# Kernel optimization log

Hardware: AMD Instinct MI355X
Metric: run time of the kernel (lower is better)

The kernel has to match this reference:

```python
import jax, jax.numpy as jnp
import numpy as np

B, D, H, W, T, C = 2, 16, 16, 16, 16, 96
NH = 4                      # num_heads
WS = (4, 4, 4, 4)           # window size
SS = (2, 2, 2, 2)           # shift size
EPS = 1e-5
HIDDEN = 4 * C


def _compute_mask():
    # Standard Swin shifted-window attention mask, extended to 4D.
    img = np.zeros((D, H, W, T), np.float32)
    sl = [[slice(0, -WS[i]), slice(-WS[i], -SS[i]), slice(-SS[i], None)] for i in range(4)]
    cnt = 0
    for a in sl[0]:
        for b in sl[1]:
            for c in sl[2]:
                for d in sl[3]:
                    img[a, b, c, d] = cnt
                    cnt += 1
    x = img.reshape(D // WS[0], WS[0], H // WS[1], WS[1], W // WS[2], WS[2], T // WS[3], WS[3])
    x = x.transpose(0, 2, 4, 6, 1, 3, 5, 7).reshape(-1, WS[0] * WS[1] * WS[2] * WS[3])
    diff = x[:, None, :] - x[:, :, None]
    return np.where(diff != 0, np.float32(-100.0), np.float32(0.0))


def setup_inputs() -> dict:
    key = jax.random.key(0)
    ks = jax.random.split(key, 6)
    w = lambda k, shape: jax.random.normal(k, shape, jnp.float32) * 0.02
    return {
        'x': jax.random.normal(ks[0], (B, D, H, W, T, C), jnp.float32),
        'mask_matrix': jnp.asarray(_compute_mask()),
        'norm1_g': jnp.ones((C,), jnp.float32), 'norm1_b': jnp.zeros((C,), jnp.float32),
        'qkv_w': w(ks[1], (3 * C, C)), 'qkv_b': jnp.zeros((3 * C,), jnp.float32),
        'proj_w': w(ks[2], (C, C)), 'proj_b': jnp.zeros((C,), jnp.float32),
        'norm2_g': jnp.ones((C,), jnp.float32), 'norm2_b': jnp.zeros((C,), jnp.float32),
        'fc1_w': w(ks[3], (HIDDEN, C)), 'fc1_b': jnp.zeros((HIDDEN,), jnp.float32),
        'fc2_w': w(ks[4], (C, HIDDEN)), 'fc2_b': jnp.zeros((C,), jnp.float32),
    }


def _ln(x, g, b):
    mu = jnp.mean(x, -1, keepdims=True)
    var = jnp.var(x, -1, keepdims=True)
    return (x - mu) * jax.lax.rsqrt(var + EPS) * g + b


def _partition(x):
    # (B, D, H, W, T, C) -> (B*nw, N, C)
    b, c = x.shape[0], x.shape[-1]
    x = x.reshape(b, D // WS[0], WS[0], H // WS[1], WS[1], W // WS[2], WS[2], T // WS[3], WS[3], c)
    x = x.transpose(0, 1, 3, 5, 7, 2, 4, 6, 8, 9)
    return x.reshape(-1, WS[0] * WS[1] * WS[2] * WS[3], c)


def _reverse(win, b):
    c = win.shape[-1]
    x = win.reshape(b, D // WS[0], H // WS[1], W // WS[2], T // WS[3], WS[0], WS[1], WS[2], WS[3], c)
    x = x.transpose(0, 1, 5, 2, 6, 3, 7, 4, 8, 9)
    return x.reshape(b, D, H, W, T, c)


def reference(x, mask_matrix, norm1_g, norm1_b, qkv_w, qkv_b, proj_w, proj_b,
              norm2_g, norm2_b, fc1_w, fc1_b, fc2_w, fc2_b):
    b, c = x.shape[0], x.shape[-1]
    hd = c // NH
    scale = hd ** -0.5
    shortcut = x
    # norm -> (no pad needed: dims divisible by window) -> cyclic shift
    xn = _ln(x, norm1_g, norm1_b)
    xs = jnp.roll(xn, shift=(-SS[0], -SS[1], -SS[2], -SS[3]), axis=(1, 2, 3, 4))
    win = _partition(xs)                              # (B_, N, C)
    B_, N, _ = win.shape
    qkv = (win @ qkv_w.T + qkv_b).reshape(B_, N, 3, NH, hd).transpose(2, 0, 3, 1, 4)
    q, k, v = qkv[0] * scale, qkv[1], qkv[2]          # (B_, NH, N, hd)
    attn = jnp.einsum('bhid,bhjd->bhij', q, k)        # (B_, NH, N, N)
    nw = mask_matrix.shape[0]
    attn = attn.reshape(B_ // nw, nw, NH, N, N) + mask_matrix[None, :, None]
    attn = jax.nn.softmax(attn.reshape(B_, NH, N, N), axis=-1)
    out = jnp.einsum('bhij,bhjd->bhid', attn, v)
    out = out.transpose(0, 2, 1, 3).reshape(B_, N, c)
    out = out @ proj_w.T + proj_b
    xr = _reverse(out, b)
    xr = jnp.roll(xr, shift=SS, axis=(1, 2, 3, 4))    # reverse cyclic shift
    x = shortcut + xr
    # MLP block
    h = _ln(x, norm2_g, norm2_b)
    h = jax.nn.gelu(h @ fc1_w.T + fc1_b, approximate=False)
    return x + (h @ fc2_w.T + fc2_b)
```

## Files before the change

kernel.cpp:

```cpp
#include <hip/hip_runtime.h>

#define TOK   131072
#define BWIN  512

typedef __attribute__((ext_vector_type(8))) short bf16x8;
typedef __attribute__((ext_vector_type(4))) float f32x4;

__device__ __forceinline__ unsigned short f2us(float f) {
  union { float f; unsigned int i; } x; x.f = f;
  return (unsigned short)((x.i + 0x7fffu + ((x.i >> 16) & 1u)) >> 16);
}
__device__ __forceinline__ unsigned cvtpk(float lo, float hi) {
  unsigned r;
  asm("v_cvt_pk_bf16_f32 %0, %1, %2" : "=v"(r) : "v"(lo), "v"(hi));
  return r;
}

#define IW1   0
#define IW2   36864
#define IQKV  73728
#define IPROJ 104448
#define IMG_SHORTS 116736

__global__ __launch_bounds__(256) void k_prepw(
    const float* __restrict__ fc1_w, const float* __restrict__ fc2_w,
    const float* __restrict__ qkv_w, const float* __restrict__ proj_w,
    unsigned short* __restrict__ img) {
  int i = blockIdx.x * 256 + threadIdx.x;
  const int l = (i >> 3) & 63, j = i & 7;
  const int quad = l >> 4, l15 = l & 15;
  float v = 0.f;
  if (i < 36864) {
    int f = i >> 9; int nc = f / 18, rem = f - nc * 18;
    int ks = rem / 6, nt = rem - ks * 6;
    v = fc1_w[(size_t)(nc * 96 + nt * 16 + l15) * 96 + ks * 32 + quad * 8 + j];
  } else if (i < 73728) {
    int f = (i - 36864) >> 9; int nc = f / 18, rem = f - nc * 18;
    int ks = rem / 6, nt = rem - ks * 6;
    v = fc2_w[(size_t)(nt * 16 + l15) * 384 + nc * 96 + ks * 32 + quad * 8 + j];
  } else if (i < 104448) {
    int f = (i - 73728) >> 9; int h = f / 15, rem = f - h * 15;
    int ks = rem / 5, mt = rem - ks * 5;
    int e = mt * 16 + l15;
    if (e < 72) {
      int grp = e / 24, rr = e - grp * 24;
      v = qkv_w[(size_t)(grp * 96 + h * 24 + rr) * 96 + ks * 32 + quad * 8 + j];
    }
  } else {
    int f = (i - 104448) >> 9; int h = f / 6, nt = f - h * 6;
    int e = quad * 8 + j;
    if (e < 24) v = proj_w[(size_t)(nt * 16 + l15) * 96 + h * 24 + e];
  }
  img[i] = f2us(v);
}

__global__ __launch_bounds__(256) void k_ln1(const float* __restrict__ x,
                                             const float* __restrict__ g,
                                             const float* __restrict__ b,
                                             unsigned short* __restrict__ xn) {
  const int wave = threadIdx.x >> 6, lane = threadIdx.x & 63;
  const int t = blockIdx.x * 4 + wave;
  const int b_ = t >> 8, n = t & 255;
  const int batch = b_ >> 8, wi = b_ & 255;
  const int wd = (wi >> 6) & 3, wh = (wi >> 4) & 3, ww = (wi >> 2) & 3, wt = wi & 3;
  const int aa = (n >> 6) & 3, bb = (n >> 4) & 3, cc = (n >> 2) & 3, dd = n & 3;
  const int sd = (wd * 4 + aa + 2) & 15, sh = (wh * 4 + bb + 2) & 15;
  const int sw = (ww * 4 + cc + 2) & 15, st = (wt * 4 + dd + 2) & 15;
  const size_t gg = ((((size_t)(batch * 16 + sd) * 16 + sh) * 16 + sw) * 16 + st);

  float2 f;
  if (lane < 48) f = *(const float2*)(x + gg * 96 + 2 * lane);
  else { f.x = 0.f; f.y = 0.f; }
  float s = f.x + f.y, q2 = f.x * f.x + f.y * f.y;
  #pragma unroll
  for (int m = 1; m < 64; m <<= 1) { s += __shfl_xor(s, m, 64); q2 += __shfl_xor(q2, m, 64); }
  const float mu = s * (1.f / 96.f);
  const float var = q2 * (1.f / 96.f) - mu * mu;
  const float rs = rsqrtf(fmaxf(var, 0.f) + 1e-5f);
  if (lane < 48) {
    float a0 = (f.x - mu) * rs * g[2 * lane]     + b[2 * lane];
    float a1 = (f.y - mu) * rs * g[2 * lane + 1] + b[2 * lane + 1];
    ((unsigned int*)xn)[(size_t)t * 48 + lane] = cvtpk(a0, a1);
  }
}

#define O_K   10240
#define O_VT  20480
#define O_U   28928
#define O_LB  37632
#define LDS_BYTES 75520

__global__ __launch_bounds__(256, 2) void k_win(
    const unsigned short* __restrict__ xn, const float* __restrict__ x,
    const unsigned short* __restrict__ img,
    const float* __restrict__ qkv_b, const float* __restrict__ proj_b,
    float* __restrict__ out) {
  extern __shared__ short lds[];
  short* s_q  = lds;
  short* s_k  = lds + O_K;
  short* s_vt = lds + O_VT;
  short* s_u  = lds + O_U;
  unsigned char* s_lb = (unsigned char*)(lds + O_LB);

  const int tid = threadIdx.x;
  const int w = tid >> 6, l = tid & 63, quad = l >> 4, l15 = l & 15;
  const int q0 = w * 64;
  const int b_ = blockIdx.x;
  const int batch = b_ >> 8, wi = b_ & 255;
  const int wd = (wi >> 6) & 3, wh = (wi >> 4) & 3, ww = (wi >> 2) & 3, wt = wi & 3;
  const float scale = 0.20412414523193154f;
  const f32x4 fz = {0.f, 0.f, 0.f, 0.f};

  {
    const int n = tid;
    const int aa = (n >> 6) & 3, bb = (n >> 4) & 3, cc = (n >> 2) & 3, dd = n & 3;
    const int p0 = wd * 4 + aa, p1 = wh * 4 + bb, p2 = ww * 4 + cc, p3 = wt * 4 + dd;
    const int r0 = p0 >= 14 ? 2 : (p0 >= 12 ? 1 : 0);
    const int r1 = p1 >= 14 ? 2 : (p1 >= 12 ? 1 : 0);
    const int r2 = p2 >= 14 ? 2 : (p2 >= 12 ? 1 : 0);
    const int r3 = p3 >= 14 ? 2 : (p3 >= 12 ? 1 : 0);
    s_lb[n] = (unsigned char)(((r0 * 3 + r1) * 3 + r2) * 3 + r3);
    unsigned int* qp = (unsigned int*)(s_q + n * 40 + 24);
    unsigned int* kp = (unsigned int*)(s_k + n * 40 + 24);
    #pragma unroll
    for (int i = 0; i < 8; i++) { qp[i] = 0u; kp[i] = 0u; }
    unsigned int* vz = (unsigned int*)(s_vt + 24 * 264);
    for (int i = tid; i < 8 * 132; i += 256)
      vz[i] = (i < 132) ? 0x3f803f80u : 0u;
  }
  __syncthreads();

  unsigned lj4[16];
  #pragma unroll
  for (int km = 0; km < 16; km++)
    lj4[km] = *(const unsigned*)&s_lb[km * 16 + quad * 4];

  f32x4 pacc[4][6];
  #pragma unroll
  for (int mt = 0; mt < 4; mt++)
    #pragma unroll
    for (int nt = 0; nt < 6; nt++) pacc[mt][nt] = fz;

  const unsigned short* xw = xn + (size_t)b_ * 256 * 96;
  const unsigned short* wq = img + IQKV;
  const unsigned short* wp = img + IPROJ;

  for (int h = 0; h < 4; h++) {
    f32x4 acc[5][4];
    #pragma unroll
    for (int mt = 0; mt < 5; mt++)
      #pragma unroll
      for (int nt = 0; nt < 4; nt++) acc[mt][nt] = fz;
    #pragma unroll
    for (int ks = 0; ks < 3; ks++) {
      bf16x8 aw[5];
      #pragma unroll
      for (int mt = 0; mt < 5; mt++)
        aw[mt] = *(const bf16x8*)(wq + ((h * 3 + ks) * 5 + mt) * 512 + l * 8);
      #pragma unroll
      for (int nt = 0; nt < 4; nt++) {
        bf16x8 bx = *(const bf16x8*)(xw + (size_t)(q0 + nt * 16 + l15) * 96 + ks * 32 + quad * 8);
        #pragma unroll
        for (int mt = 0; mt < 5; mt++)
          acc[mt][nt] = __builtin_amdgcn_mfma_f32_16x16x32_bf16(aw[mt], bx, acc[mt][nt], 0, 0, 0);
      }
    }
    #pragma unroll
    for (int mt = 0; mt < 5; mt++) {
      const int e0 = mt * 16 + quad * 4;
      #pragma unroll
      for (int nt = 0; nt < 4; nt++) {
        const int tok = q0 + nt * 16 + l15;
        if (e0 < 24) {
          uint2 pk;
          pk.x = cvtpk((acc[mt][nt][0] + qkv_b[h * 24 + e0]) * scale,
                       (acc[mt][nt][1] + qkv_b[h * 24 + e0 + 1]) * scale);
          pk.y = cvtpk((acc[mt][nt][2] + qkv_b[h * 24 + e0 + 2]) * scale,
                       (acc[mt][nt][3] + qkv_b[h * 24 + e0 + 3]) * scale);
          *(uint2*)&s_q[tok * 40 + e0] = pk;
        } else if (e0 < 48) {
          const int e = e0 - 24;
          uint2 pk;
          pk.x = cvtpk(acc[mt][nt][0] + qkv_b[96 + h * 24 + e],
                       acc[mt][nt][1] + qkv_b[96 + h * 24 + e + 1]);
          pk.y = cvtpk(acc[mt][nt][2] + qkv_b[96 + h * 24 + e + 2],
                       acc[mt][nt][3] + qkv_b[96 + h * 24 + e + 3]);
          *(uint2*)&s_k[tok * 40 + e] = pk;
        } else if (e0 < 72) {
          const int e = e0 - 48;
          #pragma unroll
          for (int r = 0; r < 4; r++)
            s_vt[(e + r) * 264 + tok] = (short)f2us(acc[mt][nt][r] + qkv_b[192 + h * 24 + e + r]);
        }
      }
    }
    __syncthreads();
    short* s_p = s_u + w * 2176;
    #pragma unroll 1
    for (int mt4 = 0; mt4 < 4; mt4++) {
      const int qt0 = q0 + mt4 * 16;
      f32x4 sc[16];
      #pragma unroll
      for (int km = 0; km < 16; km++) sc[km] = fz;
      bf16x8 bq = *(const bf16x8*)&s_q[(qt0 + l15) * 40 + quad * 8];
      __builtin_amdgcn_s_setprio(1);
      #pragma unroll
      for (int km = 0; km < 16; km++) {
        bf16x8 ak = *(const bf16x8*)&s_k[(km * 16 + l15) * 40 + quad * 8];
        sc[km] = __builtin_amdgcn_mfma_f32_16x16x32_bf16(ak, bq, sc[km], 0, 0, 0);
      }
      __builtin_amdgcn_s_setprio(0);
      const unsigned lq = s_lb[qt0 + l15];
      f32x4 ov[2] = {fz, fz};
      #pragma unroll
      for (int half = 0; half < 2; half++) {
        asm volatile("s_waitcnt lgkmcnt(0)" ::: "memory");
        #pragma unroll
        for (int km = half * 8; km < half * 8 + 8; km++) {
          unsigned lj = lj4[km];
          float p0 = ((lj & 255u)         == lq) ? __expf(sc[km][0]) : 0.f;
          float p1 = (((lj >> 8) & 255u)  == lq) ? __expf(sc[km][1]) : 0.f;
          float p2 = (((lj >> 16) & 255u) == lq) ? __expf(sc[km][2]) : 0.f;
          float p3 = ((lj >> 24)          == lq) ? __expf(sc[km][3]) : 0.f;
          uint2 pk;
          pk.x = cvtpk(p0, p1);
          pk.y = cvtpk(p2, p3);
          *(uint2*)&s_p[l15 * 136 + (km - half * 8) * 16 + quad * 4] = pk;
        }
        asm volatile("s_waitcnt lgkmcnt(0)" ::: "memory");
        __builtin_amdgcn_s_setprio(1);
        #pragma unroll
        for (int ks = 0; ks < 4; ks++) {
          bf16x8 bp = *(const bf16x8*)&s_p[l15 * 136 + ks * 32 + quad * 8];
          #pragma unroll
          for (int vm = 0; vm < 2; vm++) {
            bf16x8 av = *(const bf16x8*)&s_vt[(vm * 16 + l15) * 264 + half * 128 + ks * 32 + quad * 8];
            ov[vm] = __builtin_amdgcn_mfma_f32_16x16x32_bf16(av, bp, ov[vm], 0, 0, 0);
          }
        }
        __builtin_amdgcn_s_setprio(0);
      }
      float rsum = __shfl(ov[1][0], 32 + l15, 64);
      float inv = 1.f / rsum;
      uint2 o0;
      o0.x = cvtpk(ov[0][0] * inv, ov[0][1] * inv);
      o0.y = cvtpk(ov[0][2] * inv, ov[0][3] * inv);
      *(uint2*)&s_q[(qt0 + l15) * 40 + quad * 4] = o0;
      if (quad < 2) {
        uint2 o1;
        o1.x = cvtpk(ov[1][0] * inv, ov[1][1] * inv);
        o1.y = cvtpk(ov[1][2] * inv, ov[1][3] * inv);
        *(uint2*)&s_q[(qt0 + l15) * 40 + 16 + quad * 4] = o1;
      }
    }
    {
      bf16x8 bp[6];
      #pragma unroll
      for (int nt = 0; nt < 6; nt++)
        bp[nt] = *(const bf16x8*)(wp + (h * 6 + nt) * 512 + l * 8);
      #pragma unroll
      for (int mt = 0; mt < 4; mt++) {
        bf16x8 ao = *(const bf16x8*)&s_q[(q0 + mt * 16 + l15) * 40 + quad * 8];
        #pragma unroll
        for (int nt = 0; nt < 6; nt++)
          pacc[mt][nt] = __builtin_amdgcn_mfma_f32_16x16x32_bf16(ao, bp[nt], pacc[mt][nt], 0, 0, 0);
      }
    }
    __syncthreads();
  }

  #pragma unroll
  for (int mt = 0; mt < 4; mt++) {
    #pragma unroll
    for (int r = 0; r < 4; r++) {
      int n = q0 + mt * 16 + quad * 4 + r;
      const int aa = (n >> 6) & 3, bb = (n >> 4) & 3, cc = (n >> 2) & 3, dd = n & 3;
      const int sd = (wd * 4 + aa + 2) & 15, sh = (wh * 4 + bb + 2) & 15;
      const int sw = (ww * 4 + cc + 2) & 15, st = (wt * 4 + dd + 2) & 15;
      const size_t gg = ((((size_t)(batch * 16 + sd) * 16 + sh) * 16 + sw) * 16 + st);
      #pragma unroll
      for (int nt = 0; nt < 6; nt++) {
        int c = nt * 16 + l15;
        out[gg * 96 + c] = x[gg * 96 + c] + proj_b[c] + pacc[mt][nt][r];
      }
    }
  }
}

__global__ __launch_bounds__(256, 3) void k_mlp(
    float* __restrict__ io,
    const float* __restrict__ n2g, const float* __restrict__ n2b,
    const unsigned short* __restrict__ img,
    const float* __restrict__ fc1_b, const float* __restrict__ fc2_b) {
  __shared__ __align__(16) short s_a[128 * 104];
  __shared__ __align__(16) short s_h[128 * 104];

  const int tid = threadIdx.x;
  const int w = tid >> 6, l = tid & 63;
  const int quad = l >> 4, l15 = l & 15;
  const size_t t0 = (size_t)blockIdx.x * 128;
  const f32x4 fz = {0.f, 0.f, 0.f, 0.f};

  {
    const int r = tid >> 1, hf = tid & 1;
    const float4* base = (const float4*)(io + (t0 + r) * 96 + hf * 48);
    float v[48];
    float s = 0.f, q = 0.f;
    #pragma unroll
    for (int j = 0; j < 12; j++) {
      float4 f = base[j];
      v[4 * j] = f.x; v[4 * j + 1] = f.y; v[4 * j + 2] = f.z; v[4 * j + 3] = f.w;
      s += f.x + f.y + f.z + f.w;
      q += f.x * f.x + f.y * f.y + f.z * f.z + f.w * f.w;
    }
    s += __shfl_xor(s, 1); q += __shfl_xor(q, 1);
    const float mu = s * (1.f / 96.f);
    const float var = q * (1.f / 96.f) - mu * mu;
    const float rs = rsqrtf(fmaxf(var, 0.f) + 1e-5f);
    unsigned int* row = (unsigned int*)&s_a[r * 104] + hf * 24;
    #pragma unroll
    for (int jj = 0; jj < 24; jj++) {
      int k0 = hf * 48 + 2 * jj;
      float lo = (v[2 * jj]     - mu) * rs * n2g[k0]     + n2b[k0];
      float hi = (v[2 * jj + 1] - mu) * rs * n2g[k0 + 1] + n2b[k0 + 1];
      row[jj] = cvtpk(lo, hi);
    }
  }

  f32x4 acc2[2][6];
  #pragma unroll
  for (int m = 0; m < 2; m++)
    #pragma unroll
    for (int i = 0; i < 6; i++) acc2[m][i] = fz;

  for (int nc = 0; nc < 4; nc++) {
    f32x4 acc1[2][6];
    #pragma unroll
    for (int m = 0; m < 2; m++)
      #pragma unroll
      for (int i = 0; i < 6; i++) acc1[m][i] = fz;
    #pragma unroll
    for (int ks = 0; ks < 3; ks++) {
      bf16x8 bw[6];
      #pragma unroll
      for (int nt = 0; nt < 6; nt++)
        bw[nt] = *(const bf16x8*)(img + IW1 + ((nc * 3 + ks) * 6 + nt) * 512 + l * 8);
      #pragma unroll
      for (int m = 0; m < 2; m++) {
        bf16x8 af = *(const bf16x8*)&s_a[(w * 32 + m * 16 + l15) * 104 + ks * 32 + quad * 8];
        #pragma unroll
        for (int nt = 0; nt < 6; nt++)
          acc1[m][nt] = __builtin_amdgcn_mfma_f32_16x16x32_bf16(af, bw[nt], acc1[m][nt], 0, 0, 0);
      }
    }
    #pragma unroll
    for (int m = 0; m < 2; m++)
      #pragma unroll
      for (int nt = 0; nt < 6; nt++) {
        int col = nt * 16 + l15;
        float bv = fc1_b[nc * 96 + col];
        #pragma unroll
        for (int r = 0; r < 4; r++) {
          float z = acc1[m][nt][r] + bv;
          float g = 0.5f * z * (1.f + erff(z * 0.70710678118654752f));
          s_h[(w * 32 + m * 16 + quad * 4 + r) * 104 + col] = (short)f2us(g);
        }
      }
    #pragma unroll
    for (int ks = 0; ks < 3; ks++) {
      bf16x8 bw[6];
      #pragma unroll
      for (int nt = 0; nt < 6; nt++)
        bw[nt] = *(const bf16x8*)(img + IW2 + ((nc * 3 + ks) * 6 + nt) * 512 + l * 8);
      #pragma unroll
      for (int m = 0; m < 2; m++) {
        bf16x8 af = *(const bf16x8*)&s_h[(w * 32 + m * 16 + l15) * 104 + ks * 32 + quad * 8];
        #pragma unroll
        for (int nt = 0; nt < 6; nt++)
          acc2[m][nt] = __builtin_amdgcn_mfma_f32_16x16x32_bf16(af, bw[nt], acc2[m][nt], 0, 0, 0);
      }
    }
  }

  #pragma unroll
  for (int m = 0; m < 2; m++)
    #pragma unroll
    for (int nt = 0; nt < 6; nt++) {
      int col = nt * 16 + l15;
      float bv = fc2_b[col];
      #pragma unroll
      for (int r = 0; r < 4; r++) {
        size_t idx = (t0 + w * 32 + m * 16 + quad * 4 + r) * 96 + col;
        io[idx] = io[idx] + acc2[m][nt][r] + bv;
      }
    }
}

extern "C" void kernel_launch(void* const* d_in, const int* in_sizes, int n_in,
                              void* d_out, int out_size, void* d_ws, size_t ws_size,
                              hipStream_t stream) {
  const float* x      = (const float*)d_in[0];
  const float* n1g    = (const float*)d_in[2];
  const float* n1b    = (const float*)d_in[3];
  const float* qkv_w  = (const float*)d_in[4];
  const float* qkv_b  = (const float*)d_in[5];
  const float* proj_w = (const float*)d_in[6];
  const float* proj_b = (const float*)d_in[7];
  const float* n2g    = (const float*)d_in[8];
  const float* n2b    = (const float*)d_in[9];
  const float* fc1_w  = (const float*)d_in[10];
  const float* fc1_b  = (const float*)d_in[11];
  const float* fc2_w  = (const float*)d_in[12];
  const float* fc2_b  = (const float*)d_in[13];
  float* out = (float*)d_out;

  char* ws = (char*)d_ws;
  unsigned short* xn  = (unsigned short*)ws;
  unsigned short* img = (unsigned short*)(ws + 25165824u);

  (void)hipFuncSetAttribute((const void*)k_win,
                            hipFuncAttributeMaxDynamicSharedMemorySize, LDS_BYTES);
  k_prepw<<<IMG_SHORTS / 256, 256, 0, stream>>>(fc1_w, fc2_w, qkv_w, proj_w, img);
  k_ln1<<<TOK / 4, 256, 0, stream>>>(x, n1g, n1b, xn);
  k_win<<<BWIN, 256, LDS_BYTES, stream>>>(xn, x, img, qkv_b, proj_b, out);
  k_mlp<<<TOK / 128, 256, 0, stream>>>(out, n2g, n2b, img, fc1_b, fc2_b);
}
```

Baseline: 339.5 us.

## Keep Q and softmax probabilities in registers and shrink attention LDS footprint

The window attention kernel now keeps the scaled Q fragments and the softmax probabilities in registers. It uses 16x16x16 MFMAs so the accumulator layout feeds straight into the next matmul, instead of round-tripping through LDS. The row sum is computed with shuffles, which removes the ones-row trick in V^T. The projection is done per 16-row tile through a small scratch buffer, and LDS shrinks to static arrays so more blocks can be resident. LayerNorm-1 now has two threads per token with float4 loads instead of a whole wave per token, which cuts wasted lanes and shuffle work. The register-resident softmax raises register pressure, and the smaller MFMA shape issues twice as many instructions.

```diff
diff --git a/kernel.cpp b/kernel.cpp
--- a/kernel.cpp
+++ b/kernel.cpp
@@ -4,6 +4,7 @@
 #define BWIN  512
 
 typedef __attribute__((ext_vector_type(8))) short bf16x8;
+typedef __attribute__((ext_vector_type(4))) short bf16x4;
 typedef __attribute__((ext_vector_type(4))) float f32x4;
 
 __device__ __forceinline__ unsigned short f2us(float f) {
@@ -15,6 +16,7 @@
   asm("v_cvt_pk_bf16_f32 %0, %1, %2" : "=v"(r) : "v"(lo), "v"(hi));
   return r;
 }
+union U8 { uint2 u; bf16x4 v; };
 
 #define IW1   0
 #define IW2   36864
@@ -58,8 +60,8 @@
                                              const float* __restrict__ g,
                                              const float* __restrict__ b,
                                              unsigned short* __restrict__ xn) {
-  const int wave = threadIdx.x >> 6, lane = threadIdx.x & 63;
-  const int t = blockIdx.x * 4 + wave;
+  const int r = threadIdx.x >> 1, hf = threadIdx.x & 1;
+  const int t = blockIdx.x * 128 + r;
   const int b_ = t >> 8, n = t & 255;
   const int batch = b_ >> 8, wi = b_ & 255;
   const int wd = (wi >> 6) & 3, wh = (wi >> 4) & 3, ww = (wi >> 2) & 3, wt = wi & 3;
@@ -68,39 +70,39 @@
   const int sw = (ww * 4 + cc + 2) & 15, st = (wt * 4 + dd + 2) & 15;
   const size_t gg = ((((size_t)(batch * 16 + sd) * 16 + sh) * 16 + sw) * 16 + st);
 
-  float2 f;
-  if (lane < 48) f = *(const float2*)(x + gg * 96 + 2 * lane);
-  else { f.x = 0.f; f.y = 0.f; }
-  float s = f.x + f.y, q2 = f.x * f.x + f.y * f.y;
-  #pragma unroll
-  for (int m = 1; m < 64; m <<= 1) { s += __shfl_xor(s, m, 64); q2 += __shfl_xor(q2, m, 64); }
+  const float4* base = (const float4*)(x + gg * 96 + hf * 48);
+  float v[48];
+  float s = 0.f, q2 = 0.f;
+  #pragma unroll
+  for (int j = 0; j < 12; j++) {
+    float4 f = base[j];
+    v[4 * j] = f.x; v[4 * j + 1] = f.y; v[4 * j + 2] = f.z; v[4 * j + 3] = f.w;
+    s += f.x + f.y + f.z + f.w;
+    q2 += f.x * f.x + f.y * f.y + f.z * f.z + f.w * f.w;
+  }
+  s += __shfl_xor(s, 1); q2 += __shfl_xor(q2, 1);
   const float mu = s * (1.f / 96.f);
   const float var = q2 * (1.f / 96.f) - mu * mu;
   const float rs = rsqrtf(fmaxf(var, 0.f) + 1e-5f);
-  if (lane < 48) {
-    float a0 = (f.x - mu) * rs * g[2 * lane]     + b[2 * lane];
-    float a1 = (f.y - mu) * rs * g[2 * lane + 1] + b[2 * lane + 1];
-    ((unsigned int*)xn)[(size_t)t * 48 + lane] = cvtpk(a0, a1);
-  }
-}
-
-#define O_K   10240
-#define O_VT  20480
-#define O_U   28928
-#define O_LB  37632
-#define LDS_BYTES 75520
+  unsigned int* row = (unsigned int*)xn + (size_t)t * 48 + hf * 24;
+  #pragma unroll
+  for (int jj = 0; jj < 24; jj++) {
+    int k0 = hf * 48 + 2 * jj;
+    float a0 = (v[2 * jj]     - mu) * rs * g[k0]     + b[k0];
+    float a1 = (v[2 * jj + 1] - mu) * rs * g[k0 + 1] + b[k0 + 1];
+    row[jj] = cvtpk(a0, a1);
+  }
+}
 
 __global__ __launch_bounds__(256, 2) void k_win(
     const unsigned short* __restrict__ xn, const float* __restrict__ x,
     const unsigned short* __restrict__ img,
     const float* __restrict__ qkv_b, const float* __restrict__ proj_b,
     float* __restrict__ out) {
-  extern __shared__ short lds[];
-  short* s_q  = lds;
-  short* s_k  = lds + O_K;
-  short* s_vt = lds + O_VT;
-  short* s_u  = lds + O_U;
-  unsigned char* s_lb = (unsigned char*)(lds + O_LB);
+  __shared__ __align__(16) short s_k[256 * 36];
+  __shared__ __align__(16) short s_vt[32 * 260];
+  __shared__ __align__(16) short s_scr[4 * 640];
+  __shared__ unsigned char s_lb[256];
 
   const int tid = threadIdx.x;
   const int w = tid >> 6, l = tid & 63, quad = l >> 4, l15 = l & 15;
@@ -120,13 +122,10 @@
     const int r2 = p2 >= 14 ? 2 : (p2 >= 12 ? 1 : 0);
     const int r3 = p3 >= 14 ? 2 : (p3 >= 12 ? 1 : 0);
     s_lb[n] = (unsigned char)(((r0 * 3 + r1) * 3 + r2) * 3 + r3);
-    unsigned int* qp = (unsigned int*)(s_q + n * 40 + 24);
-    unsigned int* kp = (unsigned int*)(s_k + n * 40 + 24);
-    #pragma unroll
-    for (int i = 0; i < 8; i++) { qp[i] = 0u; kp[i] = 0u; }
-    unsigned int* vz = (unsigned int*)(s_vt + 24 * 264);
-    for (int i = tid; i < 8 * 132; i += 256)
-      vz[i] = (i < 132) ? 0x3f803f80u : 0u;
+    *(uint2*)&s_k[n * 36 + 24] = make_uint2(0u, 0u);
+    *(uint2*)&s_k[n * 36 + 28] = make_uint2(0u, 0u);
+    unsigned int* vz = (unsigned int*)(s_vt + 24 * 260);
+    for (int i = tid; i < 8 * 130; i += 256) vz[i] = 0u;
   }
   __syncthreads();
 
@@ -165,106 +164,101 @@
           acc[mt][nt] = __builtin_amdgcn_mfma_f32_16x16x32_bf16(aw[mt], bx, acc[mt][nt], 0, 0, 0);
       }
     }
-    #pragma unroll
-    for (int mt = 0; mt < 5; mt++) {
+    U8 qq[2][4];
+    #pragma unroll
+    for (int mt = 0; mt < 2; mt++) {
+      const int e0 = mt * 16 + quad * 4;
+      float b0 = qkv_b[h * 24 + e0],     b1 = qkv_b[h * 24 + e0 + 1];
+      float b2 = qkv_b[h * 24 + e0 + 2], b3 = qkv_b[h * 24 + e0 + 3];
+      #pragma unroll
+      for (int nt = 0; nt < 4; nt++) {
+        qq[mt][nt].u.x = cvtpk((acc[mt][nt][0] + b0) * scale, (acc[mt][nt][1] + b1) * scale);
+        qq[mt][nt].u.y = cvtpk((acc[mt][nt][2] + b2) * scale, (acc[mt][nt][3] + b3) * scale);
+      }
+    }
+    #pragma unroll
+    for (int mt = 1; mt < 5; mt++) {
       const int e0 = mt * 16 + quad * 4;
       #pragma unroll
       for (int nt = 0; nt < 4; nt++) {
         const int tok = q0 + nt * 16 + l15;
-        if (e0 < 24) {
-          uint2 pk;
-          pk.x = cvtpk((acc[mt][nt][0] + qkv_b[h * 24 + e0]) * scale,
-                       (acc[mt][nt][1] + qkv_b[h * 24 + e0 + 1]) * scale);
-          pk.y = cvtpk((acc[mt][nt][2] + qkv_b[h * 24 + e0 + 2]) * scale,
-                       (acc[mt][nt][3] + qkv_b[h * 24 + e0 + 3]) * scale);
-          *(uint2*)&s_q[tok * 40 + e0] = pk;
-        } else if (e0 < 48) {
+        if (e0 >= 24 && e0 < 48) {
           const int e = e0 - 24;
           uint2 pk;
           pk.x = cvtpk(acc[mt][nt][0] + qkv_b[96 + h * 24 + e],
                        acc[mt][nt][1] + qkv_b[96 + h * 24 + e + 1]);
           pk.y = cvtpk(acc[mt][nt][2] + qkv_b[96 + h * 24 + e + 2],
                        acc[mt][nt][3] + qkv_b[96 + h * 24 + e + 3]);
-          *(uint2*)&s_k[tok * 40 + e] = pk;
-        } else if (e0 < 72) {
+          *(uint2*)&s_k[tok * 36 + e] = pk;
+        } else if (e0 >= 48 && e0 < 72) {
           const int e = e0 - 48;
           #pragma unroll
           for (int r = 0; r < 4; r++)
-            s_vt[(e + r) * 264 + tok] = (short)f2us(acc[mt][nt][r] + qkv_b[192 + h * 24 + e + r]);
+            s_vt[(e + r) * 260 + tok] = (short)f2us(acc[mt][nt][r] + qkv_b[192 + h * 24 + e + r]);
         }
       }
     }
     __syncthreads();
-    short* s_p = s_u + w * 2176;
+    bf16x8 bpw[6];
+    #pragma unroll
+    for (int nt = 0; nt < 6; nt++)
+      bpw[nt] = *(const bf16x8*)(wp + (h * 6 + nt) * 512 + l * 8);
+    short* scr = s_scr + w * 640;
     #pragma unroll 1
     for (int mt4 = 0; mt4 < 4; mt4++) {
       const int qt0 = q0 + mt4 * 16;
       f32x4 sc[16];
       #pragma unroll
       for (int km = 0; km < 16; km++) sc[km] = fz;
-      bf16x8 bq = *(const bf16x8*)&s_q[(qt0 + l15) * 40 + quad * 8];
+      const bf16x4 bq0 = qq[0][mt4].v, bq1 = qq[1][mt4].v;
       __builtin_amdgcn_s_setprio(1);
       #pragma unroll
       for (int km = 0; km < 16; km++) {
-        bf16x8 ak = *(const bf16x8*)&s_k[(km * 16 + l15) * 40 + quad * 8];
-        sc[km] = __builtin_amdgcn_mfma_f32_16x16x32_bf16(ak, bq, sc[km], 0, 0, 0);
+        bf16x4 ak0 = *(const bf16x4*)&s_k[(km * 16 + l15) * 36 + quad * 4];
+        bf16x4 ak1 = *(const bf16x4*)&s_k[(km * 16 + l15) * 36 + 16 + quad * 4];
+        sc[km] = __builtin_amdgcn_mfma_f32_16x16x16bf16_1k(ak0, bq0, sc[km], 0, 0, 0);
+        sc[km] = __builtin_amdgcn_mfma_f32_16x16x16bf16_1k(ak1, bq1, sc[km], 0, 0, 0);
       }
       __builtin_amdgcn_s_setprio(0);
       const unsigned lq = s_lb[qt0 + l15];
-      f32x4 ov[2] = {fz, fz};
-      #pragma unroll
-      for (int half = 0; half < 2; half++) {
-        asm volatile("s_waitcnt lgkmcnt(0)" ::: "memory");
-        #pragma unroll
-        for (int km = half * 8; km < half * 8 + 8; km++) {
-          unsigned lj = lj4[km];
-          float p0 = ((lj & 255u)         == lq) ? __expf(sc[km][0]) : 0.f;
-          float p1 = (((lj >> 8) & 255u)  == lq) ? __expf(sc[km][1]) : 0.f;
-          float p2 = (((lj >> 16) & 255u) == lq) ? __expf(sc[km][2]) : 0.f;
-          float p3 = ((lj >> 24)          == lq) ? __expf(sc[km][3]) : 0.f;
-          uint2 pk;
-          pk.x = cvtpk(p0, p1);
-          pk.y = cvtpk(p2, p3);
-          *(uint2*)&s_p[l15 * 136 + (km - half * 8) * 16 + quad * 4] = pk;
-        }
-        asm volatile("s_waitcnt lgkmcnt(0)" ::: "memory");
-        __builtin_amdgcn_s_setprio(1);
-        #pragma unroll
-        for (int ks = 0; ks < 4; ks++) {
-          bf16x8 bp = *(const bf16x8*)&s_p[l15 * 136 + ks * 32 + quad * 8];
-          #pragma unroll
-          for (int vm = 0; vm < 2; vm++) {
-            bf16x8 av = *(const bf16x8*)&s_vt[(vm * 16 + l15) * 264 + half * 128 + ks * 32 + quad * 8];
-            ov[vm] = __builtin_amdgcn_mfma_f32_16x16x32_bf16(av, bp, ov[vm], 0, 0, 0);
-          }
-        }
-        __builtin_amdgcn_s_setprio(0);
-      }
-      float rsum = __shfl(ov[1][0], 32 + l15, 64);
-      float inv = 1.f / rsum;
-      uint2 o0;
-      o0.x = cvtpk(ov[0][0] * inv, ov[0][1] * inv);
-      o0.y = cvtpk(ov[0][2] * inv, ov[0][3] * inv);
-      *(uint2*)&s_q[(qt0 + l15) * 40 + quad * 4] = o0;
-      if (quad < 2) {
-        uint2 o1;
-        o1.x = cvtpk(ov[1][0] * inv, ov[1][1] * inv);
-        o1.y = cvtpk(ov[1][2] * inv, ov[1][3] * inv);
-        *(uint2*)&s_q[(qt0 + l15) * 40 + 16 + quad * 4] = o1;
-      }
-    }
-    {
-      bf16x8 bp[6];
+      float rsum = 0.f;
+      #pragma unroll
+      for (int km = 0; km < 16; km++) {
+        unsigned lj = lj4[km];
+        float p0 = ((lj & 255u)         == lq) ? __expf(sc[km][0]) : 0.f;
+        float p1 = (((lj >> 8) & 255u)  == lq) ? __expf(sc[km][1]) : 0.f;
+        float p2 = (((lj >> 16) & 255u) == lq) ? __expf(sc[km][2]) : 0.f;
+        float p3 = ((lj >> 24)          == lq) ? __expf(sc[km][3]) : 0.f;
+        sc[km][0] = p0; sc[km][1] = p1; sc[km][2] = p2; sc[km][3] = p3;
+        rsum += (p0 + p1) + (p2 + p3);
+      }
+      rsum += __shfl_xor(rsum, 16, 64);
+      rsum += __shfl_xor(rsum, 32, 64);
+      const float inv = 1.f / rsum;
+      f32x4 ov0 = fz, ov1 = fz;
+      __builtin_amdgcn_s_setprio(1);
+      #pragma unroll
+      for (int km = 0; km < 16; km++) {
+        U8 bp;
+        bp.u.x = cvtpk(sc[km][0], sc[km][1]);
+        bp.u.y = cvtpk(sc[km][2], sc[km][3]);
+        bf16x4 av0 = *(const bf16x4*)&s_vt[l15 * 260 + km * 16 + quad * 4];
+        bf16x4 av1 = *(const bf16x4*)&s_vt[(16 + l15) * 260 + km * 16 + quad * 4];
+        ov0 = __builtin_amdgcn_mfma_f32_16x16x16bf16_1k(av0, bp.v, ov0, 0, 0, 0);
+        ov1 = __builtin_amdgcn_mfma_f32_16x16x16bf16_1k(av1, bp.v, ov1, 0, 0, 0);
+      }
+      __builtin_amdgcn_s_setprio(0);
+      uint2 o0, o1;
+      o0.x = cvtpk(ov0[0] * inv, ov0[1] * inv);
+      o0.y = cvtpk(ov0[2] * inv, ov0[3] * inv);
+      o1.x = cvtpk(ov1[0] * inv, ov1[1] * inv);
+      o1.y = cvtpk(ov1[2] * inv, ov1[3] * inv);
+      *(uint2*)&scr[l15 * 40 + quad * 4] = o0;
+      *(uint2*)&scr[l15 * 40 + 16 + quad * 4] = o1;
+      bf16x8 ao = *(const bf16x8*)&scr[l15 * 40 + quad * 8];
       #pragma unroll
       for (int nt = 0; nt < 6; nt++)
-        bp[nt] = *(const bf16x8*)(wp + (h * 6 + nt) * 512 + l * 8);
-      #pragma unroll
-      for (int mt = 0; mt < 4; mt++) {
-        bf16x8 ao = *(const bf16x8*)&s_q[(q0 + mt * 16 + l15) * 40 + quad * 8];
-        #pragma unroll
-        for (int nt = 0; nt < 6; nt++)
-          pacc[mt][nt] = __builtin_amdgcn_mfma_f32_16x16x32_bf16(ao, bp[nt], pacc[mt][nt], 0, 0, 0);
-      }
+        pacc[mt4][nt] = __builtin_amdgcn_mfma_f32_16x16x32_bf16(ao, bpw[nt], pacc[mt4][nt], 0, 0, 0);
     }
     __syncthreads();
   }
@@ -418,10 +412,8 @@
   unsigned short* xn  = (unsigned short*)ws;
   unsigned short* img = (unsigned short*)(ws + 25165824u);
 
-  (void)hipFuncSetAttribute((const void*)k_win,
-                            hipFuncAttributeMaxDynamicSharedMemorySize, LDS_BYTES);
   k_prepw<<<IMG_SHORTS / 256, 256, 0, stream>>>(fc1_w, fc2_w, qkv_w, proj_w, img);
-  k_ln1<<<TOK / 4, 256, 0, stream>>>(x, n1g, n1b, xn);
-  k_win<<<BWIN, 256, LDS_BYTES, stream>>>(xn, x, img, qkv_b, proj_b, out);
+  k_ln1<<<TOK / 128, 256, 0, stream>>>(x, n1g, n1b, xn);
+  k_win<<<BWIN, 256, 0, stream>>>(xn, x, img, qkv_b, proj_b, out);
   k_mlp<<<TOK / 128, 256, 0, stream>>>(out, n2g, n2b, img, fc1_b, fc2_b);
 }
```

Measured after the change: 351.6 us. 1.04x slower.
